# Kernel tuning notes

Measured on AMD Instinct MI355X. Metric: run time of the kernel, lower is better.

## Reference

```python
import jax, jax.numpy as jnp
import numpy as np

NUM_NODES = 50000
NUM_EDGES = 1600000
IN_DIM = 128
OUT_DIM = 128
BATCH = 2


def setup_inputs() -> dict:
    key = jax.random.key(0)
    k1, k2, k3 = jax.random.split(key, 3)
    inputs = jax.random.normal(k1, (BATCH, NUM_NODES, IN_DIM), dtype=jnp.float32)
    W = jax.random.normal(k2, (IN_DIM, OUT_DIM), dtype=jnp.float32) * 0.02
    bias = jnp.zeros((1, 1, OUT_DIM), dtype=jnp.float32)
    adjacency_list = jax.random.randint(k3, (NUM_EDGES, 2), 0, NUM_NODES, dtype=jnp.int32)
    return {"inputs": inputs, "W": W, "bias": bias, "adjacency_list": adjacency_list}


def reference(inputs, W, bias, adjacency_list):
    # inputs: (B, N, Din); adjacency_list: (E, 2) with [:,0]=src, [:,1]=dst
    N = inputs.shape[1]
    src = adjacency_list[:, 0]
    dst = adjacency_list[:, 1]
    # symmetric-normalization weights, as computed in __init__
    deg = jnp.bincount(src, length=N)                      # (N,)
    node_w = jnp.sqrt(1.0 / (deg.astype(inputs.dtype) + 1.0))  # (N,)
    edge_w = node_w[src] * node_w[dst]                     # (E,)
    # dense projection (no activation: activation=None)
    x = jnp.einsum('bnd,do->bno', inputs, W)               # (B, N, Dout)
    # gather by edge source, scale by edge weight
    gathered = x[:, src, :] * edge_w[None, :, None]        # (B, E, Dout)
    # scatter-add into destination nodes (unsorted_segment_sum)
    agg = jnp.zeros_like(x).at[:, dst, :].add(gathered)    # (B, N, Dout)
    # self-loop term + aggregated neighbors + bias
    out = (node_w ** 2)[None, :, None] * x + agg + bias
    return out
```

## Files before the change

### kernel.cpp

```cpp
#include <hip/hip_runtime.h>
#include <hip/hip_bf16.h>


#define NN 50000
#define EE 1600000
#define DD 128
#define BB 2
#define NB 128
#define CHUNK 12500
#define HS 50000
#define HW4 (HS / 4)

#define GEMM_BLOCKS 391
#define SCAT_BLOCKS 782

typedef __attribute__((ext_vector_type(8))) short short8;
typedef __attribute__((ext_vector_type(8))) unsigned short ushort8v;
typedef __attribute__((ext_vector_type(4))) float floatx4;

__device__ inline unsigned short f2bf(float f) {
    unsigned u = __float_as_uint(f);
    unsigned r = u + 0x7fffu + ((u >> 16) & 1u);
    return (unsigned short)(r >> 16);
}
__device__ inline float bf2f(unsigned short h) {
    return __uint_as_float(((unsigned)h) << 16);
}

__global__ __launch_bounds__(1024) void phist_kernel(const int4* __restrict__ adj2,
                                                     unsigned int* __restrict__ histD32,
                                                     unsigned int* __restrict__ histS32,
                                                     unsigned char* __restrict__ rank) {
    __shared__ unsigned int h[HW4];
    int b = blockIdx.x;
    int p0 = b * (CHUNK / 2);

    for (int i = threadIdx.x; i < HW4; i += 1024) h[i] = 0;
    __syncthreads();
    if (blockIdx.y == 0) {
        for (int i = threadIdx.x; i < CHUNK / 2; i += 1024) {
            int4 two = adj2[p0 + i];
            unsigned ka = (unsigned)two.y, kb = (unsigned)two.w;
            unsigned sha = (ka & 3u) << 3, shb = (kb & 3u) << 3;
            unsigned olda = atomicAdd(&h[ka >> 2], 1u << sha);
            unsigned oldb = atomicAdd(&h[kb >> 2], 1u << shb);
            unsigned r0 = (olda >> sha) & 0xffu;
            unsigned r1 = (oldb >> shb) & 0xffu;
            int e = b * CHUNK + 2 * i;
            *(unsigned short*)(rank + e) = (unsigned short)(r0 | (r1 << 8));
        }
        __syncthreads();
        for (int i = threadIdx.x; i < HW4; i += 1024) histD32[(size_t)b * HW4 + i] = h[i];
    } else {
        for (int i = threadIdx.x; i < CHUNK / 2; i += 1024) {
            int4 two = adj2[p0 + i];
            unsigned ka = (unsigned)two.x, kb = (unsigned)two.z;
            atomicAdd(&h[ka >> 2], 1u << ((ka & 3u) << 3));
            atomicAdd(&h[kb >> 2], 1u << ((kb & 3u) << 3));
        }
        __syncthreads();
        for (int i = threadIdx.x; i < HW4; i += 1024) histS32[(size_t)b * HW4 + i] = h[i];
    }
}

__global__ __launch_bounds__(256) void reduce_hist_kernel(unsigned char* __restrict__ histD,
                                                          const unsigned char* __restrict__ histS,
                                                          unsigned char* __restrict__ deg8,
                                                          float* __restrict__ node_w,
                                                          int* __restrict__ blocksum) {
    int k = blockIdx.x * 256 + threadIdx.x;
    unsigned run = 0;
    if (k < NN) {
#pragma unroll 8
        for (int b = 0; b < NB; ++b) {
            size_t idx = (size_t)b * HS + k;
            unsigned c = histD[idx];
            histD[idx] = (unsigned char)run;
            run += c;
        }
        deg8[k] = (unsigned char)run;

        unsigned s = 0;
#pragma unroll 8
        for (int b = 0; b < NB; ++b) s += histS[(size_t)b * HS + k];
        node_w[k] = rsqrtf((float)s + 1.0f);
    }
    __shared__ int red[256];
    red[threadIdx.x] = (int)run;
    __syncthreads();
    for (int s2 = 128; s2 > 0; s2 >>= 1) {
        if (threadIdx.x < s2) red[threadIdx.x] += red[threadIdx.x + s2];
        __syncthreads();
    }
    if (threadIdx.x == 0) blocksum[blockIdx.x] = red[0];
}

__global__ __launch_bounds__(256) void offsets_kernel(const unsigned char* __restrict__ deg8,
                                                      const int* __restrict__ blocksum,
                                                      int* __restrict__ offsets) {
    __shared__ int base_s;
    __shared__ int s[256];
    int bid = blockIdx.x;
    if (threadIdx.x < 64) {
        int v = 0;
        for (int i = threadIdx.x; i < bid; i += 64) v += blocksum[i];
#pragma unroll
        for (int o = 32; o > 0; o >>= 1) v += __shfl_down(v, o);
        if (threadIdx.x == 0) base_s = v;
    }
    int t = bid * 256 + threadIdx.x;
    int d = (t < NN) ? deg8[t] : 0;
    s[threadIdx.x] = d;
    __syncthreads();
    for (int off = 1; off < 256; off <<= 1) {
        int v = (threadIdx.x >= off) ? s[threadIdx.x - off] : 0;
        __syncthreads();
        s[threadIdx.x] += v;
        __syncthreads();
    }
    if (t < NN) offsets[t] = base_s + s[threadIdx.x] - d;
}

#define WT_STRIDE 136
__global__ __launch_bounds__(1024) void scatter_gemm_kernel(
    const int4* __restrict__ adj2, const unsigned short* __restrict__ rank16,
    const unsigned char* __restrict__ histD, const int* __restrict__ offsets,
    unsigned short* __restrict__ csr_src,
    const float* __restrict__ in, const float* __restrict__ W,
    const float* __restrict__ node_w, unsigned short* __restrict__ y) {
    int bx = blockIdx.x;
    int gq = bx / 3, r = bx - 3 * gq;
    if (r != 0) {
        int i = (2 * gq + r - 1) * 1024 + threadIdx.x;
        if (i < EE / 2) {
            int4 two = adj2[i];
            unsigned rr = rank16[i];
            int e = 2 * i;
            int b = e / CHUNK;
            int posA = offsets[two.y] + (int)histD[(size_t)b * HS + two.y] + (int)(rr & 0xffu);
            int posB = offsets[two.w] + (int)histD[(size_t)b * HS + two.w] + (int)(rr >> 8);
            csr_src[posA] = (unsigned short)two.x;
            csr_src[posB] = (unsigned short)two.z;
        }
        return;
    }
    __shared__ unsigned short wt[128 * WT_STRIDE];
    for (int i = threadIdx.x; i < 128 * 128; i += 1024) {
        int d = i >> 7, o = i & 127;
        wt[o * WT_STRIDE + d] = f2bf(W[i]);
    }
    __syncthreads();

    int wave = threadIdx.x >> 6;
    int lane = threadIdx.x & 63;
    int m = lane & 15;
    int quad = lane >> 4;
    int rt = (gq * 16 + wave) * 16;
    if (rt >= BB * NN) return;

    short8 a[4];
    const float* arow = in + (size_t)(rt + m) * 128;
#pragma unroll
    for (int kt = 0; kt < 4; ++kt) {
        int k0 = kt * 32 + quad * 8;
        float4 f0 = *(const float4*)(arow + k0);
        float4 f1 = *(const float4*)(arow + k0 + 4);
        short8 av;
        av[0] = (short)f2bf(f0.x); av[1] = (short)f2bf(f0.y);
        av[2] = (short)f2bf(f0.z); av[3] = (short)f2bf(f0.w);
        av[4] = (short)f2bf(f1.x); av[5] = (short)f2bf(f1.y);
        av[6] = (short)f2bf(f1.z); av[7] = (short)f2bf(f1.w);
        a[kt] = av;
    }

    float nw[4];
#pragma unroll
    for (int rr = 0; rr < 4; ++rr) {
        int row = rt + quad * 4 + rr;
        int n = row - (row >= NN ? NN : 0);
        nw[rr] = node_w[n];
    }

#pragma unroll
    for (int ct = 0; ct < 8; ++ct) {
        floatx4 acc = {0.f, 0.f, 0.f, 0.f};
#pragma unroll
        for (int kt = 0; kt < 4; ++kt) {
            const short8* bp =
                (const short8*)&wt[(ct * 16 + m) * WT_STRIDE + kt * 32 + quad * 8];
            acc = __builtin_amdgcn_mfma_f32_16x16x32_bf16(a[kt], *bp, acc, 0, 0, 0);
        }
        int col = ct * 16 + m;
#pragma unroll
        for (int rr = 0; rr < 4; ++rr) {
            int row = rt + quad * 4 + rr;
            y[(size_t)row * 128 + col] = f2bf(nw[rr] * acc[rr]);
        }
    }
}

__global__ __launch_bounds__(256, 8) void aggregate_kernel(
    const unsigned short* __restrict__ yb, const unsigned short* __restrict__ csr_src,
    const int* __restrict__ offsets, const unsigned char* __restrict__ deg8,
    const float* __restrict__ node_w, const float* __restrict__ bias,
    float* __restrict__ out) {
    int wave = threadIdx.x >> 6;
    int lane = threadIdx.x & 63;
    unsigned blk = blockIdx.x;
    int xcd = (int)(blk & 7u);
    int bg = xcd >> 2;
    int nbid = (int)(blk >> 3) * 4 + (xcd & 3);
    int n = nbid * 4 + wave;

    int g = lane >> 4;
    int c8 = lane & 15;
    int c16 = c8 * 16;
    const char* ybase = (const char*)yb + (size_t)bg * (NN * 128 * 2);

    int start = __builtin_amdgcn_readfirstlane(offsets[n]);
    int cnt = __builtin_amdgcn_readfirstlane((int)deg8[n]);

    float acc[8];
#pragma unroll
    for (int k = 0; k < 8; ++k) acc[k] = 0.f;

    for (int base = 0; base < cnt; base += 64) {
        int mm = cnt - base; if (mm > 64) mm = 64;
        int v = (lane < mm) ? (int)csr_src[start + base + lane] : 0x7fffffff;
#pragma unroll
        for (int k = 2; k <= 64; k <<= 1) {
#pragma unroll
            for (int j = k >> 1; j > 0; j >>= 1) {
                int other = __shfl_xor(v, j);
                bool lower = (lane & j) == 0;
                bool up = (lane & k) == 0;
                int mn = other < v ? other : v;
                int mx = other < v ? v : other;
                v = up ? (lower ? mn : mx) : (lower ? mx : mn);
            }
        }
        int sv = v << 8;
        int j = 0;
        for (; j + 16 <= mm; j += 16) {
            int o0 = __shfl(sv, j + g) + c16;
            int o1 = __shfl(sv, j + 4 + g) + c16;
            int o2 = __shfl(sv, j + 8 + g) + c16;
            int o3 = __shfl(sv, j + 12 + g) + c16;
            ushort8v ld0 = *(const ushort8v*)(ybase + (unsigned)o0);
            ushort8v ld1 = *(const ushort8v*)(ybase + (unsigned)o1);
            ushort8v ld2 = *(const ushort8v*)(ybase + (unsigned)o2);
            ushort8v ld3 = *(const ushort8v*)(ybase + (unsigned)o3);
#pragma unroll
            for (int k = 0; k < 8; ++k) acc[k] += bf2f((unsigned short)ld0[k]);
#pragma unroll
            for (int k = 0; k < 8; ++k) acc[k] += bf2f((unsigned short)ld1[k]);
#pragma unroll
            for (int k = 0; k < 8; ++k) acc[k] += bf2f((unsigned short)ld2[k]);
#pragma unroll
            for (int k = 0; k < 8; ++k) acc[k] += bf2f((unsigned short)ld3[k]);
        }
        for (; j + 8 <= mm; j += 8) {
            int o0 = __shfl(sv, j + g) + c16;
            int o1 = __shfl(sv, j + 4 + g) + c16;
            ushort8v ld0 = *(const ushort8v*)(ybase + (unsigned)o0);
            ushort8v ld1 = *(const ushort8v*)(ybase + (unsigned)o1);
#pragma unroll
            for (int k = 0; k < 8; ++k) acc[k] += bf2f((unsigned short)ld0[k]);
#pragma unroll
            for (int k = 0; k < 8; ++k) acc[k] += bf2f((unsigned short)ld1[k]);
        }
        if (j < mm) {
            int i0 = j + g, i1 = j + 4 + g;
            int o0 = __shfl(sv, i0 < mm ? i0 : 0) + c16;
            int o1 = __shfl(sv, i1 < mm ? i1 : 0) + c16;
            if (i0 < mm) {
                ushort8v ld0 = *(const ushort8v*)(ybase + (unsigned)o0);
#pragma unroll
                for (int k = 0; k < 8; ++k) acc[k] += bf2f((unsigned short)ld0[k]);
            }
            if (i1 < mm) {
                ushort8v ld1 = *(const ushort8v*)(ybase + (unsigned)o1);
#pragma unroll
                for (int k = 0; k < 8; ++k) acc[k] += bf2f((unsigned short)ld1[k]);
            }
        }
    }

#pragma unroll
    for (int k = 0; k < 8; ++k) {
        acc[k] += __shfl_xor(acc[k], 16);
        acc[k] += __shfl_xor(acc[k], 32);
    }

    if (g == 0) {
        float nw = node_w[n];
        const unsigned short* ys = yb + (size_t)bg * (NN * 128) + (size_t)n * 128 + c8 * 8;
        ushort8v yv = *(const ushort8v*)ys;
        floatx4 o0, o1;
        const float* bp = bias + c8 * 8;
        o0.x = nw * (acc[0] + bf2f((unsigned short)yv[0])) + bp[0];
        o0.y = nw * (acc[1] + bf2f((unsigned short)yv[1])) + bp[1];
        o0.z = nw * (acc[2] + bf2f((unsigned short)yv[2])) + bp[2];
        o0.w = nw * (acc[3] + bf2f((unsigned short)yv[3])) + bp[3];
        o1.x = nw * (acc[4] + bf2f((unsigned short)yv[4])) + bp[4];
        o1.y = nw * (acc[5] + bf2f((unsigned short)yv[5])) + bp[5];
        o1.z = nw * (acc[6] + bf2f((unsigned short)yv[6])) + bp[6];
        o1.w = nw * (acc[7] + bf2f((unsigned short)yv[7])) + bp[7];
        float* op = out + ((size_t)bg * NN + n) * 128 + c8 * 8;
        __builtin_nontemporal_store(o0, (floatx4*)op);
        __builtin_nontemporal_store(o1, (floatx4*)(op + 4));
    }
}

extern "C" void kernel_launch(void* const* d_in, const int* in_sizes, int n_in,
                              void* d_out, int out_size, void* d_ws, size_t ws_size,
                              hipStream_t stream) {
    const float* inputs = (const float*)d_in[0];
    const float* W      = (const float*)d_in[1];
    const float* bias   = (const float*)d_in[2];
    const int*   adj    = (const int*)d_in[3];
    float* out = (float*)d_out;

    char* ws = (char*)d_ws;
    size_t off = 0;
    unsigned short* y = (unsigned short*)(ws + off);
    off += (size_t)BB * NN * DD * sizeof(unsigned short);
    unsigned char* histD = (unsigned char*)(ws + off);
    off += (size_t)NB * HS;
    unsigned char* histS = (unsigned char*)(ws + off);
    off += (size_t)NB * HS;
    unsigned short* csr_src = (unsigned short*)histS;
    unsigned char* rank = (unsigned char*)(ws + off);
    off += (size_t)EE;
    unsigned char* deg8 = (unsigned char*)(ws + off);
    off += (size_t)((NN + 255) & ~255);
    float* node_w = (float*)(ws + off);  off += (size_t)NN * sizeof(float);
    int* offsets = (int*)(ws + off);     off += (size_t)NN * sizeof(int);
    int* blocksum = (int*)(ws + off);    off += 256 * sizeof(int);

    dim3 hgrid(NB, 2);
    phist_kernel<<<hgrid, 1024, 0, stream>>>((const int4*)adj, (unsigned int*)histD,
                                             (unsigned int*)histS, rank);
    reduce_hist_kernel<<<(NN + 255) / 256, 256, 0, stream>>>(histD, histS, deg8, node_w,
                                                             blocksum);
    offsets_kernel<<<(NN + 255) / 256, 256, 0, stream>>>(deg8, blocksum, offsets);
    scatter_gemm_kernel<<<GEMM_BLOCKS + SCAT_BLOCKS, 1024, 0, stream>>>(
        (const int4*)adj, (const unsigned short*)rank, histD, offsets, csr_src,
        inputs, W, node_w, y);
    aggregate_kernel<<<NN / 4 * BB, 256, 0, stream>>>(y, csr_src, offsets, deg8, node_w, bias,
                                                      out);
}
```

Measured before the change: 267.9 us.

## Fuse preprocessing and GEMM stages into one cooperative kernel with grid syncs

Merges histogram, histogram reduction, offset scan and the scatter/GEMM stage into a single cooperative mega-kernel separated by grid-wide syncs. The aim is to remove three kernel launches and the gaps between them. The block-level reduction is replaced by per-wave partial sums written to a new workspace array. Each stage now runs grid-stride over a fixed persistent grid sized from occupancy. This adds grid-sync costs and can cut parallelism in stages whose blocks were previously independent. The old multi-kernel path is kept as a fallback if the cooperative launch fails.

```diff
diff --git a/kernel.cpp b/kernel.cpp
--- a/kernel.cpp
+++ b/kernel.cpp
@@ -1,5 +1,8 @@
 #include <hip/hip_runtime.h>
 #include <hip/hip_bf16.h>
+#include <hip/hip_cooperative_groups.h>
+
+namespace cg = cooperative_groups;
 
 
 #define NN 50000
@@ -13,6 +16,7 @@
 
 #define GEMM_BLOCKS 391
 #define SCAT_BLOCKS 782
+#define WT_STRIDE 136
 
 typedef __attribute__((ext_vector_type(8))) short short8;
 typedef __attribute__((ext_vector_type(8))) unsigned short ushort8v;
@@ -25,6 +29,180 @@
 }
 __device__ inline float bf2f(unsigned short h) {
     return __uint_as_float(((unsigned)h) << 16);
+}
+
+__global__ __launch_bounds__(1024) void mega_kernel(
+    const int4* __restrict__ adj2, unsigned int* __restrict__ histD32,
+    unsigned int* __restrict__ histS32, unsigned char* __restrict__ rank,
+    unsigned char* __restrict__ deg8, float* __restrict__ node_w,
+    int* __restrict__ offsets, int* __restrict__ wavesum,
+    unsigned short* __restrict__ csr_src,
+    const float* __restrict__ in, const float* __restrict__ W,
+    unsigned short* __restrict__ y) {
+    __shared__ unsigned int smem32[12512];
+    cg::grid_group grid = cg::this_grid();
+    const int nb = gridDim.x;
+    const int bid = blockIdx.x;
+    const int tid = threadIdx.x;
+    unsigned char* histD = (unsigned char*)histD32;
+
+    for (int v = bid; v < 2 * NB; v += nb) {
+        int b = v & (NB - 1);
+        int role = v >> 7;
+        int p0 = b * (CHUNK / 2);
+        for (int i = tid; i < HW4; i += 1024) smem32[i] = 0;
+        __syncthreads();
+        if (role == 0) {
+            for (int i = tid; i < CHUNK / 2; i += 1024) {
+                int4 two = adj2[p0 + i];
+                unsigned ka = (unsigned)two.y, kb = (unsigned)two.w;
+                unsigned sha = (ka & 3u) << 3, shb = (kb & 3u) << 3;
+                unsigned olda = atomicAdd(&smem32[ka >> 2], 1u << sha);
+                unsigned oldb = atomicAdd(&smem32[kb >> 2], 1u << shb);
+                unsigned r0 = (olda >> sha) & 0xffu;
+                unsigned r1 = (oldb >> shb) & 0xffu;
+                int e = b * CHUNK + 2 * i;
+                *(unsigned short*)(rank + e) = (unsigned short)(r0 | (r1 << 8));
+            }
+            __syncthreads();
+            for (int i = tid; i < HW4; i += 1024) histD32[(size_t)b * HW4 + i] = smem32[i];
+        } else {
+            for (int i = tid; i < CHUNK / 2; i += 1024) {
+                int4 two = adj2[p0 + i];
+                unsigned ka = (unsigned)two.x, kb = (unsigned)two.z;
+                atomicAdd(&smem32[ka >> 2], 1u << ((ka & 3u) << 3));
+                atomicAdd(&smem32[kb >> 2], 1u << ((kb & 3u) << 3));
+            }
+            __syncthreads();
+            for (int i = tid; i < HW4; i += 1024) histS32[(size_t)b * HW4 + i] = smem32[i];
+        }
+        __syncthreads();
+    }
+    grid.sync();
+
+    {
+        int k = bid * 1024 + tid;
+        unsigned run = 0;
+        if (k < NN) {
+            const unsigned char* histS = (const unsigned char*)histS32;
+#pragma unroll 8
+            for (int b = 0; b < NB; ++b) {
+                size_t idx = (size_t)b * HS + k;
+                unsigned c = histD[idx];
+                histD[idx] = (unsigned char)run;
+                run += c;
+            }
+            deg8[k] = (unsigned char)run;
+            unsigned s = 0;
+#pragma unroll 8
+            for (int b = 0; b < NB; ++b) s += histS[(size_t)b * HS + k];
+            node_w[k] = rsqrtf((float)s + 1.0f);
+        }
+        int v = (int)run;
+#pragma unroll
+        for (int o = 32; o > 0; o >>= 1) v += __shfl_down(v, o);
+        if ((tid & 63) == 0) wavesum[(bid * 1024 + tid) >> 6] = v;
+    }
+    grid.sync();
+
+    {
+        int* s = (int*)smem32;
+        for (int vb = bid; vb < (NN + 255) / 256; vb += nb) {
+            if (tid < 64) {
+                int acc = 0;
+                for (int i = tid; i < vb * 4; i += 64) acc += wavesum[i];
+#pragma unroll
+                for (int o = 32; o > 0; o >>= 1) acc += __shfl_down(acc, o);
+                if (tid == 0) s[256] = acc;
+            }
+            int t = vb * 256 + (tid & 255);
+            int d = 0;
+            if (tid < 256) {
+                d = (t < NN) ? deg8[t] : 0;
+                s[tid] = d;
+            }
+            __syncthreads();
+            for (int off = 1; off < 256; off <<= 1) {
+                int vv = 0;
+                if (tid < 256 && tid >= off) vv = s[tid - off];
+                __syncthreads();
+                if (tid < 256) s[tid] += vv;
+                __syncthreads();
+            }
+            if (tid < 256 && t < NN) offsets[t] = s[256] + s[tid] - d;
+            __syncthreads();
+        }
+    }
+    grid.sync();
+
+    {
+        unsigned short* wt = (unsigned short*)smem32;
+        for (int i = tid; i < 128 * 128; i += 1024) {
+            int d = i >> 7, o = i & 127;
+            wt[o * WT_STRIDE + d] = f2bf(W[i]);
+        }
+        __syncthreads();
+        int wave = tid >> 6;
+        int lane = tid & 63;
+        int m = lane & 15;
+        int quad = lane >> 4;
+        for (int gq = bid; gq < GEMM_BLOCKS; gq += nb) {
+            int rt = (gq * 16 + wave) * 16;
+            if (rt < BB * NN) {
+                short8 a[4];
+                const float* arow = in + (size_t)(rt + m) * 128;
+#pragma unroll
+                for (int kt = 0; kt < 4; ++kt) {
+                    int k0 = kt * 32 + quad * 8;
+                    float4 f0 = *(const float4*)(arow + k0);
+                    float4 f1 = *(const float4*)(arow + k0 + 4);
+                    short8 av;
+                    av[0] = (short)f2bf(f0.x); av[1] = (short)f2bf(f0.y);
+                    av[2] = (short)f2bf(f0.z); av[3] = (short)f2bf(f0.w);
+                    av[4] = (short)f2bf(f1.x); av[5] = (short)f2bf(f1.y);
+                    av[6] = (short)f2bf(f1.z); av[7] = (short)f2bf(f1.w);
+                    a[kt] = av;
+                }
+                float nw4[4];
+#pragma unroll
+                for (int r = 0; r < 4; ++r) {
+                    int row = rt + quad * 4 + r;
+                    int n = row - (row >= NN ? NN : 0);
+                    nw4[r] = node_w[n];
+                }
+#pragma unroll
+                for (int ct = 0; ct < 8; ++ct) {
+                    floatx4 acc = {0.f, 0.f, 0.f, 0.f};
+#pragma unroll
+                    for (int kt = 0; kt < 4; ++kt) {
+                        const short8* bp =
+                            (const short8*)&wt[(ct * 16 + m) * WT_STRIDE + kt * 32 + quad * 8];
+                        acc = __builtin_amdgcn_mfma_f32_16x16x32_bf16(a[kt], *bp, acc, 0, 0, 0);
+                    }
+                    int col = ct * 16 + m;
+#pragma unroll
+                    for (int r = 0; r < 4; ++r) {
+                        int row = rt + quad * 4 + r;
+                        y[(size_t)row * 128 + col] = f2bf(nw4[r] * acc[r]);
+                    }
+                }
+            }
+        }
+        const unsigned short* rank16 = (const unsigned short*)rank;
+        for (int vv = bid; vv < SCAT_BLOCKS; vv += nb) {
+            int i = vv * 1024 + tid;
+            if (i < EE / 2) {
+                int4 two = adj2[i];
+                unsigned rr = rank16[i];
+                int e = 2 * i;
+                int b = e / CHUNK;
+                int posA = offsets[two.y] + (int)histD[(size_t)b * HS + two.y] + (int)(rr & 0xffu);
+                int posB = offsets[two.w] + (int)histD[(size_t)b * HS + two.w] + (int)(rr >> 8);
+                csr_src[posA] = (unsigned short)two.x;
+                csr_src[posB] = (unsigned short)two.z;
+            }
+        }
+    }
 }
 
 __global__ __launch_bounds__(1024) void phist_kernel(const int4* __restrict__ adj2,
@@ -34,7 +212,6 @@
     __shared__ unsigned int h[HW4];
     int b = blockIdx.x;
     int p0 = b * (CHUNK / 2);
-
     for (int i = threadIdx.x; i < HW4; i += 1024) h[i] = 0;
     __syncthreads();
     if (blockIdx.y == 0) {
@@ -79,7 +256,6 @@
             run += c;
         }
         deg8[k] = (unsigned char)run;
-
         unsigned s = 0;
 #pragma unroll 8
         for (int b = 0; b < NB; ++b) s += histS[(size_t)b * HS + k];
@@ -121,7 +297,6 @@
     if (t < NN) offsets[t] = base_s + s[threadIdx.x] - d;
 }
 
-#define WT_STRIDE 136
 __global__ __launch_bounds__(1024) void scatter_gemm_kernel(
     const int4* __restrict__ adj2, const unsigned short* __restrict__ rank16,
     const unsigned char* __restrict__ histD, const int* __restrict__ offsets,
@@ -150,14 +325,12 @@
         wt[o * WT_STRIDE + d] = f2bf(W[i]);
     }
     __syncthreads();
-
     int wave = threadIdx.x >> 6;
     int lane = threadIdx.x & 63;
     int m = lane & 15;
     int quad = lane >> 4;
     int rt = (gq * 16 + wave) * 16;
     if (rt >= BB * NN) return;
-
     short8 a[4];
     const float* arow = in + (size_t)(rt + m) * 128;
 #pragma unroll
@@ -172,15 +345,13 @@
         av[6] = (short)f2bf(f1.z); av[7] = (short)f2bf(f1.w);
         a[kt] = av;
     }
-
-    float nw[4];
+    float nw4[4];
 #pragma unroll
     for (int rr = 0; rr < 4; ++rr) {
         int row = rt + quad * 4 + rr;
         int n = row - (row >= NN ? NN : 0);
-        nw[rr] = node_w[n];
-    }
-
+        nw4[rr] = node_w[n];
+    }
 #pragma unroll
     for (int ct = 0; ct < 8; ++ct) {
         floatx4 acc = {0.f, 0.f, 0.f, 0.f};
@@ -194,7 +365,7 @@
 #pragma unroll
         for (int rr = 0; rr < 4; ++rr) {
             int row = rt + quad * 4 + rr;
-            y[(size_t)row * 128 + col] = f2bf(nw[rr] * acc[rr]);
+            y[(size_t)row * 128 + col] = f2bf(nw4[rr] * acc[rr]);
         }
     }
 }
@@ -337,16 +508,39 @@
     float* node_w = (float*)(ws + off);  off += (size_t)NN * sizeof(float);
     int* offsets = (int*)(ws + off);     off += (size_t)NN * sizeof(int);
     int* blocksum = (int*)(ws + off);    off += 256 * sizeof(int);
-
-    dim3 hgrid(NB, 2);
-    phist_kernel<<<hgrid, 1024, 0, stream>>>((const int4*)adj, (unsigned int*)histD,
-                                             (unsigned int*)histS, rank);
-    reduce_hist_kernel<<<(NN + 255) / 256, 256, 0, stream>>>(histD, histS, deg8, node_w,
-                                                             blocksum);
-    offsets_kernel<<<(NN + 255) / 256, 256, 0, stream>>>(deg8, blocksum, offsets);
-    scatter_gemm_kernel<<<GEMM_BLOCKS + SCAT_BLOCKS, 1024, 0, stream>>>(
-        (const int4*)adj, (const unsigned short*)rank, histD, offsets, csr_src,
-        inputs, W, node_w, y);
+    int* wavesum = (int*)(ws + off);     off += 8192 * sizeof(int);
+
+    static int coop_blocks = -1;
+    if (coop_blocks < 0) {
+        int occ = 0;
+        hipError_t e = hipOccupancyMaxActiveBlocksPerMultiprocessor(&occ, mega_kernel, 1024, 0);
+        coop_blocks = (e == hipSuccess) ? occ * 256 : 0;
+        if (coop_blocks > 512) coop_blocks = 512;
+    }
+
+    bool coop_ok = coop_blocks >= 49;
+    if (coop_ok) {
+        const int4* adj2 = (const int4*)adj;
+        unsigned int* histD32 = (unsigned int*)histD;
+        unsigned int* histS32 = (unsigned int*)histS;
+        void* args[] = {(void*)&adj2,   (void*)&histD32, (void*)&histS32, (void*)&rank,
+                        (void*)&deg8,   (void*)&node_w,  (void*)&offsets, (void*)&wavesum,
+                        (void*)&csr_src,(void*)&inputs,  (void*)&W,       (void*)&y};
+        hipError_t e = hipLaunchCooperativeKernel((const void*)mega_kernel, dim3(coop_blocks),
+                                                  dim3(1024), args, 0, stream);
+        if (e != hipSuccess) coop_ok = false;
+    }
+    if (!coop_ok) {
+        dim3 hgrid(NB, 2);
+        phist_kernel<<<hgrid, 1024, 0, stream>>>((const int4*)adj, (unsigned int*)histD,
+                                                 (unsigned int*)histS, rank);
+        reduce_hist_kernel<<<(NN + 255) / 256, 256, 0, stream>>>(histD, histS, deg8, node_w,
+                                                                 blocksum);
+        offsets_kernel<<<(NN + 255) / 256, 256, 0, stream>>>(deg8, blocksum, offsets);
+        scatter_gemm_kernel<<<GEMM_BLOCKS + SCAT_BLOCKS, 1024, 0, stream>>>(
+            (const int4*)adj, (const unsigned short*)rank, histD, offsets, csr_src,
+            inputs, W, node_w, y);
+    }
     aggregate_kernel<<<NN / 4 * BB, 256, 0, stream>>>(y, csr_src, offsets, deg8, node_w, bias,
                                                       out);
 }
```

Measured after the change: 385.8 us. 44.0% more time.
